# Performance work log

Hardware: AMD Instinct MI355X
Metric: run time of the kernel (lower is better)

Reference implementation:

```python
import jax, jax.numpy as jnp
import numpy as np

N = 100000   # nodes
E = 1600000  # edges (avg degree 16)
IN, H, HID, OUT = 128, 2, 64, 32


def setup_inputs() -> dict:
    key = jax.random.key(0)
    ks = jax.random.split(key, 20)
    def p(k, shape, scale=0.1):
        return jax.random.normal(k, shape, jnp.float32) * scale
    inp = {
        "x": jax.random.normal(ks[0], (N, IN), jnp.float32),
        "edge_index": jax.random.randint(ks[1], (2, E), 0, N),
    }
    # per-layer params: W [din, H*dout], att_src/att_dst [H, dout], bias
    dims = [(IN, HID), (H * HID, HID), (H * HID, HID), (H * HID, OUT)]
    for i, (din, dout) in enumerate(dims):
        inp[f"W{i}"] = p(ks[2 + 4 * i], (din, H * dout))
        inp[f"asrc{i}"] = p(ks[3 + 4 * i], (H, dout))
        inp[f"adst{i}"] = p(ks[4 + 4 * i], (H, dout))
        inp[f"b{i}"] = jnp.zeros((H * dout if i < 3 else dout,), jnp.float32)
    return inp


def gat_conv(h, src, dst, W, a_s, a_d, b, concat):
    # PyG GATConv, add_self_loops=False, negative_slope=0.2, eval mode
    heads, dout = a_s.shape
    n = h.shape[0]
    xl = (h @ W).reshape(n, heads, dout)              # [N, H, D]
    alpha_src = jnp.einsum('nhd,hd->nh', xl, a_s)     # [N, H]
    alpha_dst = jnp.einsum('nhd,hd->nh', xl, a_d)
    e = alpha_src[src] + alpha_dst[dst]               # [E, H]
    e = jax.nn.leaky_relu(e, 0.2)
    # segment softmax over edges sharing a destination node
    m = jax.ops.segment_max(e, dst, num_segments=n)
    m = jnp.where(jnp.isfinite(m), m, 0.0)            # guard isolated nodes
    ex = jnp.exp(e - m[dst])
    denom = jax.ops.segment_sum(ex, dst, num_segments=n)
    alpha = ex / (denom[dst] + 1e-16)                 # [E, H]
    msg = xl[src] * alpha[:, :, None]                 # [E, H, D]
    out = jax.ops.segment_sum(msg, dst, num_segments=n)
    out = out.reshape(n, heads * dout) if concat else out.mean(axis=1)
    return out + b


def reference(x, edge_index, W0, asrc0, adst0, b0, W1, asrc1, adst1, b1,
              W2, asrc2, adst2, b2, W3, asrc3, adst3, b3):
    src, dst = edge_index[0], edge_index[1]
    layers = [
        (W0, asrc0, adst0, b0, True),
        (W1, asrc1, adst1, b1, True),
        (W2, asrc2, adst2, b2, True),
        (W3, asrc3, adst3, b3, False),
    ]
    h = x
    for i, (W, a_s, a_d, b, concat) in enumerate(layers):
        h = gat_conv(h, src, dst, W, a_s, a_d, b, concat)
        if i != len(layers) - 1:
            h = jax.nn.relu(h)
    return jax.nn.log_softmax(h, axis=-1)
```

## Files before the change

### kernel.cpp

```cpp
#include <hip/hip_runtime.h>
#include <hip/hip_bf16.h>
#include <math.h>

#define N_NODES 100000
#define N_EDGES 1600000

constexpr int BSHIFT = 9, BMASK = 511;
constexpr int NBUCKET = (N_NODES + 511) / 512;
constexpr int BCAP = 16384;
constexpr int CAPB = 12288;
constexpr int EPT = 16, BIN_T = 256, BIN_CHUNK = BIN_T * EPT;

typedef __attribute__((ext_vector_type(8))) short bf16x8;
typedef __attribute__((ext_vector_type(4))) float f32x4;

__device__ __forceinline__ unsigned short f2bf(float f) {
    unsigned int u = __float_as_uint(f);
    unsigned int r = (u + 0x7fff + ((u >> 16) & 1)) >> 16;
    return (unsigned short)r;
}


__global__ __launch_bounds__(BIN_T) void bin_kernel(const int* __restrict__ src,
                                                    const int* __restrict__ dst,
                                                    int* __restrict__ bcnt,
                                                    unsigned int* __restrict__ bstore, int E) {
    __shared__ int cnt[NBUCKET];
    __shared__ int base[NBUCKET];
    int t = threadIdx.x;
    for (int i = t; i < NBUCKET; i += BIN_T) cnt[i] = 0;
    __syncthreads();
    int e0 = blockIdx.x * BIN_CHUNK;
    int ssrc[EPT], sdst[EPT];
#pragma unroll
    for (int k = 0; k < EPT; ++k) {
        int e = e0 + t + k * BIN_T;
        if (e < E) {
            ssrc[k] = src[e];
            sdst[k] = dst[e];
            atomicAdd(&cnt[sdst[k] >> BSHIFT], 1);
        } else {
            sdst[k] = -1;
        }
    }
    __syncthreads();
    for (int i = t; i < NBUCKET; i += BIN_T) {
        base[i] = atomicAdd(&bcnt[i], cnt[i]);
        cnt[i] = 0;
    }
    __syncthreads();
#pragma unroll
    for (int k = 0; k < EPT; ++k) {
        if (sdst[k] >= 0) {
            int b = sdst[k] >> BSHIFT;
            int off = base[b] + atomicAdd(&cnt[b], 1);
            if (off < BCAP)
                bstore[(size_t)b * BCAP + off] =
                    ((unsigned)ssrc[k] << BSHIFT) | (unsigned)(sdst[k] & BMASK);
        }
    }
}

__global__ __launch_bounds__(256) void scan_bcnt_kernel(const int* __restrict__ bcnt,
                                                        int* __restrict__ bbase) {
    __shared__ int sh[256];
    int t = threadIdx.x;
    int v = (t < NBUCKET) ? min(bcnt[t], BCAP) : 0;
    sh[t] = v;
    __syncthreads();
    for (int off = 1; off < 256; off <<= 1) {
        int x = (t >= off) ? sh[t - off] : 0;
        __syncthreads();
        sh[t] += x;
        __syncthreads();
    }
    if (t < NBUCKET) bbase[t + 1] = sh[t];
    if (t == 0) bbase[0] = 0;
}

__global__ __launch_bounds__(256) void build_col_v2(const int* __restrict__ bcnt,
                                                    const int* __restrict__ bbase,
                                                    const unsigned int* __restrict__ bstore,
                                                    int* __restrict__ rp, int* __restrict__ col,
                                                    int N) {
    __shared__ int sA[512], sB[512];
    __shared__ int lofs[513];
    __shared__ int colStage[CAPB];
    int b = blockIdx.x, t = threadIdx.x;
    int nodeBase = b << BSHIFT;
    int nNodes = min(512, N - nodeBase);
    for (int i = t; i < 512; i += 256) sA[i] = 0;
    __syncthreads();
    int cnt = min(bcnt[b], BCAP);
    size_t sbase = (size_t)b * BCAP;
    for (int i = t; i < cnt; i += 256) atomicAdd(&sA[bstore[sbase + i] & BMASK], 1);
    __syncthreads();
    int* srcp = sA; int* dstp = sB;
    for (int off = 1; off < 512; off <<= 1) {
        for (int i = t; i < 512; i += 256) dstp[i] = srcp[i] + ((i >= off) ? srcp[i - off] : 0);
        __syncthreads();
        int* tmp = srcp; srcp = dstp; dstp = tmp;
    }
    for (int i = t; i < 512; i += 256) lofs[i + 1] = srcp[i];
    if (t == 0) lofs[0] = 0;
    for (int i = t; i < 512; i += 256) dstp[i] = 0;
    __syncthreads();
    int gbase = bbase[b];
    for (int i = t; i < nNodes; i += 256) rp[nodeBase + i] = gbase + lofs[i];
    if (b == NBUCKET - 1 && t == 0) rp[N] = gbase + lofs[nNodes];
    for (int i = t; i < cnt; i += 256) {
        unsigned e = bstore[sbase + i];
        int dl = e & BMASK;
        int sv = (int)(e >> BSHIFT);
        int pos = lofs[dl] + atomicAdd(&dstp[dl], 1);
        if (pos < CAPB) colStage[pos] = sv;
        else col[gbase + pos] = sv;
    }
    __syncthreads();
    int lim = min(cnt, CAPB);
    for (int i = t; i < lim; i += 256) col[gbase + i] = colStage[i];
}

__global__ __launch_bounds__(256) void transpose_all_w(
    const float* __restrict__ W0, const float* __restrict__ W1,
    const float* __restrict__ W2, const float* __restrict__ W3,
    unsigned int* __restrict__ Wt0, unsigned int* __restrict__ Wt1,
    unsigned int* __restrict__ Wt2, unsigned int* __restrict__ Wt3) {
    int idx = blockIdx.x * 256 + threadIdx.x;
    const float* W; unsigned int* Wt; int C, base;
    if (idx < 8192)       { W = W0; Wt = Wt0; C = 128; base = 0; }
    else if (idx < 16384) { W = W1; Wt = Wt1; C = 128; base = 8192; }
    else if (idx < 24576) { W = W2; Wt = Wt2; C = 128; base = 16384; }
    else if (idx < 28672) { W = W3; Wt = Wt3; C = 64;  base = 24576; }
    else return;
    int l = idx - base;
    int c = l >> 6, kk = l & 63;
    float w0 = W[(2 * kk) * C + c];
    float w1 = W[(2 * kk + 1) * C + c];
    Wt[c * 64 + kk] = (unsigned)f2bf(w0) | ((unsigned)f2bf(w1) << 16);
}


template<int HD, bool F32IN>
__global__ __launch_bounds__(64) void gemm_alpha_mfma(
    const void* __restrict__ hsrc, const unsigned short* __restrict__ Wt,
    const float* __restrict__ a_s, const float* __restrict__ a_d,
    __hip_bfloat16* __restrict__ xl, float* __restrict__ asrc, float* __restrict__ adst) {
    constexpr int NT = HD / 16;
    constexpr int GR = HD / 4;
    int node0 = blockIdx.x * 16;
    int t = threadIdx.x;
    int lan = t & 15, grp = t >> 4;

    __shared__ float ob[16][HD + 4];

    bf16x8 af[4];
    if constexpr (F32IN) {
        __shared__ unsigned short hb[16][136];
        const float4* h4 = (const float4*)hsrc;
#pragma unroll
        for (int it = 0; it < 8; ++it) {
            int idx = it * 64 + t;
            int nn = idx >> 5, kk = idx & 31;
            float4 v = h4[(size_t)(node0 + nn) * 32 + kk];
            ushort4 u;
            u.x = f2bf(v.x); u.y = f2bf(v.y); u.z = f2bf(v.z); u.w = f2bf(v.w);
            *(ushort4*)&hb[nn][kk * 4] = u;
        }
        __syncthreads();
#pragma unroll
        for (int ks = 0; ks < 4; ++ks)
            af[ks] = *(const bf16x8*)&hb[lan][ks * 32 + grp * 8];
    } else {
        const unsigned short* hbf = (const unsigned short*)hsrc;
#pragma unroll
        for (int ks = 0; ks < 4; ++ks)
            af[ks] = *(const bf16x8*)(hbf + (size_t)(node0 + lan) * 128 + ks * 32 + grp * 8);
    }

    f32x4 acc[NT];
#pragma unroll
    for (int i = 0; i < NT; ++i) acc[i] = (f32x4){0.f, 0.f, 0.f, 0.f};

#pragma unroll
    for (int ks = 0; ks < 4; ++ks) {
        bf16x8 bfr[NT];
#pragma unroll
        for (int nt = 0; nt < NT; ++nt)
            bfr[nt] = *(const bf16x8*)(Wt + (size_t)(nt * 16 + lan) * 128 + ks * 32 + grp * 8);
#pragma unroll
        for (int nt = 0; nt < NT; ++nt)
            acc[nt] = __builtin_amdgcn_mfma_f32_16x16x32_bf16(af[ks], bfr[nt], acc[nt], 0, 0, 0);
    }

    float av[NT], dv[NT];
#pragma unroll
    for (int nt = 0; nt < NT; ++nt) {
        av[nt] = a_s[nt * 16 + lan];
        dv[nt] = a_d[nt * 16 + lan];
    }
    float psum[2][4] = {{0.f,0.f,0.f,0.f},{0.f,0.f,0.f,0.f}};
    float pdum[2][4] = {{0.f,0.f,0.f,0.f},{0.f,0.f,0.f,0.f}};
#pragma unroll
    for (int nt = 0; nt < NT; ++nt) {
        int hs = (nt >= NT / 2) ? 1 : 0;
#pragma unroll
        for (int j = 0; j < 4; ++j) {
            psum[hs][j] = fmaf(acc[nt][j], av[nt], psum[hs][j]);
            pdum[hs][j] = fmaf(acc[nt][j], dv[nt], pdum[hs][j]);
        }
    }
#pragma unroll
    for (int off = 1; off <= 8; off <<= 1) {
#pragma unroll
        for (int hs = 0; hs < 2; ++hs)
#pragma unroll
            for (int j = 0; j < 4; ++j) {
                psum[hs][j] += __shfl_xor(psum[hs][j], off, 64);
                pdum[hs][j] += __shfl_xor(pdum[hs][j], off, 64);
            }
    }
    if (lan == 0) {
#pragma unroll
        for (int j = 0; j < 4; ++j) {
            int node = node0 + grp * 4 + j;
            asrc[node * 2 + 0] = psum[0][j];
            asrc[node * 2 + 1] = psum[1][j];
            adst[node * 2 + 0] = pdum[0][j];
            adst[node * 2 + 1] = pdum[1][j];
        }
    }

#pragma unroll
    for (int nt = 0; nt < NT; ++nt)
#pragma unroll
        for (int j = 0; j < 4; ++j)
            ob[grp * 4 + j][nt * 16 + lan] = acc[nt][j];
    __syncthreads();
#pragma unroll
    for (int it = 0; it < 16 * GR / 64; ++it) {
        int idx = it * 64 + t;
        int nn = idx / GR, g = idx % GR;
        float4 v = *(const float4*)&ob[nn][g * 4];
        uint2 u;
        u.x = (unsigned)f2bf(v.x) | ((unsigned)f2bf(v.y) << 16);
        u.y = (unsigned)f2bf(v.z) | ((unsigned)f2bf(v.w) << 16);
        ((uint2*)xl)[(size_t)(node0 + nn) * GR + g] = u;
    }
}


__global__ void aggregate_relu_v5(const __hip_bfloat162* __restrict__ xl2,
                                  const float2* __restrict__ a_src, const float2* __restrict__ a_dst,
                                  const int* __restrict__ rp, const int* __restrict__ col,
                                  const float* __restrict__ bias, unsigned int* __restrict__ out) {
    int node = blockIdx.x;
    int t = threadIdx.x;
    int head = t >> 5;
    int beg = rp[node], deg = rp[node + 1] - beg;
    float2 adn = a_dst[node];

    __shared__ int   snS[64];
    __shared__ float pS[2][64];

    float s0 = 0.f, s1 = 0.f;
    float ax0 = 0.f, ay0 = 0.f, ax1 = 0.f, ay1 = 0.f;
    float ax2 = 0.f, ay2 = 0.f, ax3 = 0.f, ay3 = 0.f;

    if (deg <= 64) {
        float e0 = -INFINITY, e1 = -INFINITY;
        if (t < deg) {
            int sn = col[beg + t];
            snS[t] = sn;
            float2 a = a_src[sn];
            e0 = a.x + adn.x; e0 = (e0 >= 0.f) ? e0 : 0.2f * e0;
            e1 = a.y + adn.y; e1 = (e1 >= 0.f) ? e1 : 0.2f * e1;
        }
        float m0 = e0, m1 = e1;
#pragma unroll
        for (int off = 32; off >= 1; off >>= 1) {
            m0 = fmaxf(m0, __shfl_xor(m0, off, 64));
            m1 = fmaxf(m1, __shfl_xor(m1, off, 64));
        }
        if (t < deg) {
            float p0 = __expf(e0 - m0), p1 = __expf(e1 - m1);
            pS[0][t] = p0; pS[1][t] = p1;
            s0 = p0; s1 = p1;
        }
        __syncthreads();
        int j = 0;
        for (; j + 8 <= deg; j += 8) {
            int sa = snS[j+0], sb = snS[j+1], sc = snS[j+2], sd = snS[j+3];
            int se = snS[j+4], sf = snS[j+5], sg = snS[j+6], sh = snS[j+7];
            float pa = pS[head][j+0], pb = pS[head][j+1], pc = pS[head][j+2], pd = pS[head][j+3];
            float pe = pS[head][j+4], pf = pS[head][j+5], pg = pS[head][j+6], ph = pS[head][j+7];
            __hip_bfloat162 va = xl2[(size_t)sa * 64 + t];
            __hip_bfloat162 vb = xl2[(size_t)sb * 64 + t];
            __hip_bfloat162 vc = xl2[(size_t)sc * 64 + t];
            __hip_bfloat162 vd = xl2[(size_t)sd * 64 + t];
            __hip_bfloat162 ve = xl2[(size_t)se * 64 + t];
            __hip_bfloat162 vf = xl2[(size_t)sf * 64 + t];
            __hip_bfloat162 vg = xl2[(size_t)sg * 64 + t];
            __hip_bfloat162 vh = xl2[(size_t)sh * 64 + t];
            ax0 = fmaf(pa, __bfloat162float(va.x), ax0); ay0 = fmaf(pa, __bfloat162float(va.y), ay0);
            ax1 = fmaf(pb, __bfloat162float(vb.x), ax1); ay1 = fmaf(pb, __bfloat162float(vb.y), ay1);
            ax2 = fmaf(pc, __bfloat162float(vc.x), ax2); ay2 = fmaf(pc, __bfloat162float(vc.y), ay2);
            ax3 = fmaf(pd, __bfloat162float(vd.x), ax3); ay3 = fmaf(pd, __bfloat162float(vd.y), ay3);
            ax0 = fmaf(pe, __bfloat162float(ve.x), ax0); ay0 = fmaf(pe, __bfloat162float(ve.y), ay0);
            ax1 = fmaf(pf, __bfloat162float(vf.x), ax1); ay1 = fmaf(pf, __bfloat162float(vf.y), ay1);
            ax2 = fmaf(pg, __bfloat162float(vg.x), ax2); ay2 = fmaf(pg, __bfloat162float(vg.y), ay2);
            ax3 = fmaf(ph, __bfloat162float(vh.x), ax3); ay3 = fmaf(ph, __bfloat162float(vh.y), ay3);
        }
        for (; j < deg; ++j) {
            int sn = snS[j];
            float p = pS[head][j];
            __hip_bfloat162 v = xl2[(size_t)sn * 64 + t];
            ax0 = fmaf(p, __bfloat162float(v.x), ax0);
            ay0 = fmaf(p, __bfloat162float(v.y), ay0);
        }
    } else {
        float m0 = -INFINITY, m1 = -INFINITY;
        for (int j = t; j < deg; j += 64) {
            float2 a = a_src[col[beg + j]];
            float e0 = a.x + adn.x; e0 = (e0 >= 0.f) ? e0 : 0.2f * e0;
            float e1 = a.y + adn.y; e1 = (e1 >= 0.f) ? e1 : 0.2f * e1;
            m0 = fmaxf(m0, e0); m1 = fmaxf(m1, e1);
        }
#pragma unroll
        for (int off = 32; off >= 1; off >>= 1) {
            m0 = fmaxf(m0, __shfl_xor(m0, off, 64));
            m1 = fmaxf(m1, __shfl_xor(m1, off, 64));
        }
        for (int c0 = 0; c0 < deg; c0 += 64) {
            int csz = min(64, deg - c0);
            if (t < csz) {
                int sn = col[beg + c0 + t];
                float2 a = a_src[sn];
                float e0 = a.x + adn.x; e0 = (e0 >= 0.f) ? e0 : 0.2f * e0;
                float e1 = a.y + adn.y; e1 = (e1 >= 0.f) ? e1 : 0.2f * e1;
                float p0 = __expf(e0 - m0), p1 = __expf(e1 - m1);
                snS[t] = sn; pS[0][t] = p0; pS[1][t] = p1;
                s0 += p0; s1 += p1;
            }
            __syncthreads();
            for (int j = 0; j < csz; ++j) {
                int sn = snS[j];
                float p = pS[head][j];
                __hip_bfloat162 v = xl2[(size_t)sn * 64 + t];
                ax0 = fmaf(p, __bfloat162float(v.x), ax0);
                ay0 = fmaf(p, __bfloat162float(v.y), ay0);
            }
            __syncthreads();
        }
    }
#pragma unroll
    for (int off = 32; off >= 1; off >>= 1) {
        s0 += __shfl_xor(s0, off, 64);
        s1 += __shfl_xor(s1, off, 64);
    }
    float s = head ? s1 : s0;
    float inv = 1.0f / (s + 1e-16f);
    float2 b2 = ((const float2*)bias)[t];
    float ox = fmaxf(fmaf(ax0 + ax1 + ax2 + ax3, inv, b2.x), 0.f);
    float oy = fmaxf(fmaf(ay0 + ay1 + ay2 + ay3, inv, b2.y), 0.f);
    out[(size_t)node * 64 + t] = (unsigned)f2bf(ox) | ((unsigned)f2bf(oy) << 16);
}

__global__ void aggregate_final_v4(const __hip_bfloat16* __restrict__ xl,
                                   const float2* __restrict__ a_src, const float2* __restrict__ a_dst,
                                   const int* __restrict__ rp, const int* __restrict__ col,
                                   const float* __restrict__ bias, float* __restrict__ out) {
    int node = blockIdx.x;
    int t = threadIdx.x;
    int head = t >> 5;
    int beg = rp[node], deg = rp[node + 1] - beg;
    float2 adn = a_dst[node];

    __shared__ int   snS[64];
    __shared__ float pS[2][64];

    float s0 = 0.f, s1 = 0.f;
    float a0 = 0.f, a1 = 0.f, a2 = 0.f, a3 = 0.f;

    if (deg <= 64) {
        float e0 = -INFINITY, e1 = -INFINITY;
        if (t < deg) {
            int sn = col[beg + t];
            snS[t] = sn;
            float2 a = a_src[sn];
            e0 = a.x + adn.x; e0 = (e0 >= 0.f) ? e0 : 0.2f * e0;
            e1 = a.y + adn.y; e1 = (e1 >= 0.f) ? e1 : 0.2f * e1;
        }
        float m0 = e0, m1 = e1;
#pragma unroll
        for (int off = 32; off >= 1; off >>= 1) {
            m0 = fmaxf(m0, __shfl_xor(m0, off, 64));
            m1 = fmaxf(m1, __shfl_xor(m1, off, 64));
        }
        if (t < deg) {
            float p0 = __expf(e0 - m0), p1 = __expf(e1 - m1);
            pS[0][t] = p0; pS[1][t] = p1;
            s0 = p0; s1 = p1;
        }
        __syncthreads();
        int j = 0;
        for (; j + 8 <= deg; j += 8) {
            int sa = snS[j+0], sb = snS[j+1], sc = snS[j+2], sd = snS[j+3];
            int se = snS[j+4], sf = snS[j+5], sg = snS[j+6], sh = snS[j+7];
            float pa = pS[head][j+0], pb = pS[head][j+1], pc = pS[head][j+2], pd = pS[head][j+3];
            float pe = pS[head][j+4], pf = pS[head][j+5], pg = pS[head][j+6], ph = pS[head][j+7];
            float va = __bfloat162float(xl[(size_t)sa * 64 + t]);
            float vb = __bfloat162float(xl[(size_t)sb * 64 + t]);
            float vc = __bfloat162float(xl[(size_t)sc * 64 + t]);
            float vd = __bfloat162float(xl[(size_t)sd * 64 + t]);
            float ve = __bfloat162float(xl[(size_t)se * 64 + t]);
            float vf = __bfloat162float(xl[(size_t)sf * 64 + t]);
            float vg = __bfloat162float(xl[(size_t)sg * 64 + t]);
            float vh = __bfloat162float(xl[(size_t)sh * 64 + t]);
            a0 = fmaf(pa, va, a0); a1 = fmaf(pb, vb, a1);
            a2 = fmaf(pc, vc, a2); a3 = fmaf(pd, vd, a3);
            a0 = fmaf(pe, ve, a0); a1 = fmaf(pf, vf, a1);
            a2 = fmaf(pg, vg, a2); a3 = fmaf(ph, vh, a3);
        }
        for (; j < deg; ++j) {
            a0 = fmaf(pS[head][j], __bfloat162float(xl[(size_t)snS[j] * 64 + t]), a0);
        }
    } else {
        float m0 = -INFINITY, m1 = -INFINITY;
        for (int j = t; j < deg; j += 64) {
            float2 a = a_src[col[beg + j]];
            float e0 = a.x + adn.x; e0 = (e0 >= 0.f) ? e0 : 0.2f * e0;
            float e1 = a.y + adn.y; e1 = (e1 >= 0.f) ? e1 : 0.2f * e1;
            m0 = fmaxf(m0, e0); m1 = fmaxf(m1, e1);
        }
#pragma unroll
        for (int off = 32; off >= 1; off >>= 1) {
            m0 = fmaxf(m0, __shfl_xor(m0, off, 64));
            m1 = fmaxf(m1, __shfl_xor(m1, off, 64));
        }
        for (int c0 = 0; c0 < deg; c0 += 64) {
            int csz = min(64, deg - c0);
            if (t < csz) {
                int sn = col[beg + c0 + t];
                float2 a = a_src[sn];
                float e0 = a.x + adn.x; e0 = (e0 >= 0.f) ? e0 : 0.2f * e0;
                float e1 = a.y + adn.y; e1 = (e1 >= 0.f) ? e1 : 0.2f * e1;
                float p0 = __expf(e0 - m0), p1 = __expf(e1 - m1);
                snS[t] = sn; pS[0][t] = p0; pS[1][t] = p1;
                s0 += p0; s1 += p1;
            }
            __syncthreads();
            for (int j = 0; j < csz; ++j) {
                a0 = fmaf(pS[head][j], __bfloat162float(xl[(size_t)snS[j] * 64 + t]), a0);
            }
            __syncthreads();
        }
    }
#pragma unroll
    for (int off = 32; off >= 1; off >>= 1) {
        s0 += __shfl_xor(s0, off, 64);
        s1 += __shfl_xor(s1, off, 64);
    }
    float s = head ? s1 : s0;
    float o = (a0 + a1 + a2 + a3) / (s + 1e-16f);
    float other = __shfl_down(o, 32, 64);
    if (t < 32) {
        float v = 0.5f * (o + other) + bias[t];
        float mx = v;
#pragma unroll
        for (int off = 16; off >= 1; off >>= 1) mx = fmaxf(mx, __shfl_xor(mx, off, 32));
        float ex = __expf(v - mx);
        float sm = ex;
#pragma unroll
        for (int off = 16; off >= 1; off >>= 1) sm += __shfl_xor(sm, off, 32);
        out[(size_t)node * 32 + t] = v - mx - logf(sm);
    }
}


extern "C" void kernel_launch(void* const* d_in, const int* in_sizes, int n_in,
                              void* d_out, int out_size, void* d_ws, size_t ws_size,
                              hipStream_t stream) {
    const int N = N_NODES, E = N_EDGES;

    const float* x  = (const float*)d_in[0];
    const int*  ei  = (const int*)d_in[1];
    const float* W0 = (const float*)d_in[2];
    const float* as0 = (const float*)d_in[3];
    const float* ad0 = (const float*)d_in[4];
    const float* b0 = (const float*)d_in[5];
    const float* W1 = (const float*)d_in[6];
    const float* as1 = (const float*)d_in[7];
    const float* ad1 = (const float*)d_in[8];
    const float* b1 = (const float*)d_in[9];
    const float* W2 = (const float*)d_in[10];
    const float* as2 = (const float*)d_in[11];
    const float* ad2 = (const float*)d_in[12];
    const float* b2 = (const float*)d_in[13];
    const float* W3 = (const float*)d_in[14];
    const float* as3 = (const float*)d_in[15];
    const float* ad3 = (const float*)d_in[16];
    const float* b3 = (const float*)d_in[17];
    float* out = (float*)d_out;

    const int* srcv = ei;
    const int* dstv = ei + E;

    char* p = (char*)d_ws;
    auto carve = [&](size_t bytes) -> void* {
        void* r = (void*)p;
        p += (bytes + 255) & ~(size_t)255;
        return r;
    };
    int* rp       = (int*)carve((size_t)(N + 1) * 4);
    int* col      = (int*)carve((size_t)E * 4);
    int* bcnt     = (int*)carve((size_t)NBUCKET * 4);
    int* bbase    = (int*)carve((size_t)(NBUCKET + 1) * 4);
    unsigned int* bstore = (unsigned int*)carve((size_t)NBUCKET * BCAP * 4);
    __hip_bfloat16* bufX = (__hip_bfloat16*)carve((size_t)N * 128 * 2);
    __hip_bfloat16* bufH = (__hip_bfloat16*)carve((size_t)N * 128 * 2);
    float* asrc   = (float*)carve((size_t)N * 2 * 4);
    float* adst   = (float*)carve((size_t)N * 2 * 4);
    unsigned short* Wt0 = (unsigned short*)carve((size_t)128 * 128 * 2);
    unsigned short* Wt1 = (unsigned short*)carve((size_t)128 * 128 * 2);
    unsigned short* Wt2 = (unsigned short*)carve((size_t)128 * 128 * 2);
    unsigned short* Wt3 = (unsigned short*)carve((size_t)64 * 128 * 2);

    hipMemsetAsync(bcnt, 0, (size_t)NBUCKET * 4, stream);

    transpose_all_w<<<112, 256, 0, stream>>>(W0, W1, W2, W3,
                                             (unsigned int*)Wt0, (unsigned int*)Wt1,
                                             (unsigned int*)Wt2, (unsigned int*)Wt3);

    bin_kernel<<<(E + BIN_CHUNK - 1) / BIN_CHUNK, BIN_T, 0, stream>>>(srcv, dstv, bcnt, bstore, E);
    scan_bcnt_kernel<<<1, 256, 0, stream>>>(bcnt, bbase);
    build_col_v2<<<NBUCKET, 256, 0, stream>>>(bcnt, bbase, bstore, rp, col, N);

    const __hip_bfloat162* bufX2 = (const __hip_bfloat162*)bufX;
    const float2* asrc2 = (const float2*)asrc;
    const float2* adst2 = (const float2*)adst;

    gemm_alpha_mfma<128, true><<<N / 16, 64, 0, stream>>>(x, Wt0, as0, ad0, bufX, asrc, adst);
    aggregate_relu_v5<<<N, 64, 0, stream>>>(bufX2, asrc2, adst2, rp, col, b0, (unsigned int*)bufH);
    gemm_alpha_mfma<128, false><<<N / 16, 64, 0, stream>>>(bufH, Wt1, as1, ad1, bufX, asrc, adst);
    aggregate_relu_v5<<<N, 64, 0, stream>>>(bufX2, asrc2, adst2, rp, col, b1, (unsigned int*)bufH);
    gemm_alpha_mfma<128, false><<<N / 16, 64, 0, stream>>>(bufH, Wt2, as2, ad2, bufX, asrc, adst);
    aggregate_relu_v5<<<N, 64, 0, stream>>>(bufX2, asrc2, adst2, rp, col, b2, (unsigned int*)bufH);
    gemm_alpha_mfma<64, false><<<N / 16, 64, 0, stream>>>(bufH, Wt3, as3, ad3, bufX, asrc, adst);
    aggregate_final_v4<<<N, 64, 0, stream>>>(bufX, asrc2, adst2, rp, col, b3, out);
}
```

Before: 532.7 us.

## Fold attention dot products into GEMM weights and merge bucket scan into column build

Precomputes W·a_src and W·a_dst per head as four extra weight columns (plus zero padding to a full MFMA tile), so the attention logits come out of one additional MFMA tile rather than a per-block FMA and shuffle reduction. Separately, the one-block bucket-count scan is folded into the column-build kernel, where every block redoes the 256-entry scan, removing one launch. The cost is an extra MFMA tile and extra weight loads per GEMM block, and the attention logits now come from bf16-rounded fused weights, which changes their precision.

Measured after the change: 557.8 us. 1.05x slower.

```diff
diff --git a/kernel.cpp b/kernel.cpp
--- a/kernel.cpp
+++ b/kernel.cpp
@@ -61,32 +61,26 @@
     }
 }
 
-__global__ __launch_bounds__(256) void scan_bcnt_kernel(const int* __restrict__ bcnt,
-                                                        int* __restrict__ bbase) {
-    __shared__ int sh[256];
-    int t = threadIdx.x;
-    int v = (t < NBUCKET) ? min(bcnt[t], BCAP) : 0;
-    sh[t] = v;
-    __syncthreads();
-    for (int off = 1; off < 256; off <<= 1) {
-        int x = (t >= off) ? sh[t - off] : 0;
-        __syncthreads();
-        sh[t] += x;
-        __syncthreads();
-    }
-    if (t < NBUCKET) bbase[t + 1] = sh[t];
-    if (t == 0) bbase[0] = 0;
-}
-
-__global__ __launch_bounds__(256) void build_col_v2(const int* __restrict__ bcnt,
-                                                    const int* __restrict__ bbase,
+__global__ __launch_bounds__(256) void build_col_v3(const int* __restrict__ bcnt,
                                                     const unsigned int* __restrict__ bstore,
                                                     int* __restrict__ rp, int* __restrict__ col,
                                                     int N) {
+    __shared__ int sc[256];
     __shared__ int sA[512], sB[512];
     __shared__ int lofs[513];
     __shared__ int colStage[CAPB];
     int b = blockIdx.x, t = threadIdx.x;
+    int v = (t < NBUCKET) ? min(bcnt[t], BCAP) : 0;
+    sc[t] = v;
+    __syncthreads();
+    for (int off = 1; off < 256; off <<= 1) {
+        int x = (t >= off) ? sc[t - off] : 0;
+        __syncthreads();
+        sc[t] += x;
+        __syncthreads();
+    }
+    int gbase = (b == 0) ? 0 : sc[b - 1];
+
     int nodeBase = b << BSHIFT;
     int nNodes = min(512, N - nodeBase);
     for (int i = t; i < 512; i += 256) sA[i] = 0;
@@ -105,7 +99,6 @@
     if (t == 0) lofs[0] = 0;
     for (int i = t; i < 512; i += 256) dstp[i] = 0;
     __syncthreads();
-    int gbase = bbase[b];
     for (int i = t; i < nNodes; i += 256) rp[nodeBase + i] = gbase + lofs[i];
     if (b == NBUCKET - 1 && t == 0) rp[N] = gbase + lofs[nNodes];
     for (int i = t; i < cnt; i += 256) {
@@ -140,11 +133,38 @@
     Wt[c * 64 + kk] = (unsigned)f2bf(w0) | ((unsigned)f2bf(w1) << 16);
 }
 
+__global__ __launch_bounds__(512) void fuse_dots(
+    const float* __restrict__ W0, const float* __restrict__ W1,
+    const float* __restrict__ W2, const float* __restrict__ W3,
+    const float* __restrict__ as0, const float* __restrict__ ad0,
+    const float* __restrict__ as1, const float* __restrict__ ad1,
+    const float* __restrict__ as2, const float* __restrict__ ad2,
+    const float* __restrict__ as3, const float* __restrict__ ad3,
+    unsigned short* __restrict__ Wt0, unsigned short* __restrict__ Wt1,
+    unsigned short* __restrict__ Wt2, unsigned short* __restrict__ Wt3) {
+    int l = blockIdx.x;
+    int t = threadIdx.x;
+    const float* W  = (l == 0) ? W0 : (l == 1) ? W1 : (l == 2) ? W2 : W3;
+    const float* as = (l == 0) ? as0 : (l == 1) ? as1 : (l == 2) ? as2 : as3;
+    const float* ad = (l == 0) ? ad0 : (l == 1) ? ad1 : (l == 2) ? ad2 : ad3;
+    unsigned short* Wt = (l == 0) ? Wt0 : (l == 1) ? Wt1 : (l == 2) ? Wt2 : Wt3;
+    int C = (l < 3) ? 128 : 64;
+    int dout = C / 2;
+    int k = t & 127, v = t >> 7;
+    int head = v & 1;
+    const float* a = (v >> 1) ? ad : as;
+    float s = 0.f;
+    for (int d = 0; d < dout; ++d)
+        s += W[k * C + head * dout + d] * a[head * dout + d];
+    Wt[(C + v) * 128 + k] = f2bf(s);
+    int padBase = (C + 4) * 128;
+    for (int i = t; i < 12 * 128; i += 512) Wt[padBase + i] = 0;
+}
+
 
 template<int HD, bool F32IN>
 __global__ __launch_bounds__(64) void gemm_alpha_mfma(
     const void* __restrict__ hsrc, const unsigned short* __restrict__ Wt,
-    const float* __restrict__ a_s, const float* __restrict__ a_d,
     __hip_bfloat16* __restrict__ xl, float* __restrict__ asrc, float* __restrict__ adst) {
     constexpr int NT = HD / 16;
     constexpr int GR = HD / 4;
@@ -178,56 +198,28 @@
             af[ks] = *(const bf16x8*)(hbf + (size_t)(node0 + lan) * 128 + ks * 32 + grp * 8);
     }
 
-    f32x4 acc[NT];
-#pragma unroll
-    for (int i = 0; i < NT; ++i) acc[i] = (f32x4){0.f, 0.f, 0.f, 0.f};
+    f32x4 acc[NT + 1];
+#pragma unroll
+    for (int i = 0; i <= NT; ++i) acc[i] = (f32x4){0.f, 0.f, 0.f, 0.f};
 
 #pragma unroll
     for (int ks = 0; ks < 4; ++ks) {
-        bf16x8 bfr[NT];
-#pragma unroll
-        for (int nt = 0; nt < NT; ++nt)
+        bf16x8 bfr[NT + 1];
+#pragma unroll
+        for (int nt = 0; nt <= NT; ++nt)
             bfr[nt] = *(const bf16x8*)(Wt + (size_t)(nt * 16 + lan) * 128 + ks * 32 + grp * 8);
 #pragma unroll
-        for (int nt = 0; nt < NT; ++nt)
+        for (int nt = 0; nt <= NT; ++nt)
             acc[nt] = __builtin_amdgcn_mfma_f32_16x16x32_bf16(af[ks], bfr[nt], acc[nt], 0, 0, 0);
     }
 
-    float av[NT], dv[NT];
-#pragma unroll
-    for (int nt = 0; nt < NT; ++nt) {
-        av[nt] = a_s[nt * 16 + lan];
-        dv[nt] = a_d[nt * 16 + lan];
-    }
-    float psum[2][4] = {{0.f,0.f,0.f,0.f},{0.f,0.f,0.f,0.f}};
-    float pdum[2][4] = {{0.f,0.f,0.f,0.f},{0.f,0.f,0.f,0.f}};
-#pragma unroll
-    for (int nt = 0; nt < NT; ++nt) {
-        int hs = (nt >= NT / 2) ? 1 : 0;
-#pragma unroll
-        for (int j = 0; j < 4; ++j) {
-            psum[hs][j] = fmaf(acc[nt][j], av[nt], psum[hs][j]);
-            pdum[hs][j] = fmaf(acc[nt][j], dv[nt], pdum[hs][j]);
-        }
-    }
-#pragma unroll
-    for (int off = 1; off <= 8; off <<= 1) {
-#pragma unroll
-        for (int hs = 0; hs < 2; ++hs)
-#pragma unroll
-            for (int j = 0; j < 4; ++j) {
-                psum[hs][j] += __shfl_xor(psum[hs][j], off, 64);
-                pdum[hs][j] += __shfl_xor(pdum[hs][j], off, 64);
-            }
-    }
-    if (lan == 0) {
+    if (lan < 4) {
+        float* dst = (lan < 2) ? asrc : adst;
+        int hh = lan & 1;
 #pragma unroll
         for (int j = 0; j < 4; ++j) {
             int node = node0 + grp * 4 + j;
-            asrc[node * 2 + 0] = psum[0][j];
-            asrc[node * 2 + 1] = psum[1][j];
-            adst[node * 2 + 0] = pdum[0][j];
-            adst[node * 2 + 1] = pdum[1][j];
+            dst[node * 2 + hh] = acc[NT][j];
         }
     }
 
@@ -515,37 +507,38 @@
     int* rp       = (int*)carve((size_t)(N + 1) * 4);
     int* col      = (int*)carve((size_t)E * 4);
     int* bcnt     = (int*)carve((size_t)NBUCKET * 4);
-    int* bbase    = (int*)carve((size_t)(NBUCKET + 1) * 4);
     unsigned int* bstore = (unsigned int*)carve((size_t)NBUCKET * BCAP * 4);
     __hip_bfloat16* bufX = (__hip_bfloat16*)carve((size_t)N * 128 * 2);
     __hip_bfloat16* bufH = (__hip_bfloat16*)carve((size_t)N * 128 * 2);
     float* asrc   = (float*)carve((size_t)N * 2 * 4);
     float* adst   = (float*)carve((size_t)N * 2 * 4);
-    unsigned short* Wt0 = (unsigned short*)carve((size_t)128 * 128 * 2);
-    unsigned short* Wt1 = (unsigned short*)carve((size_t)128 * 128 * 2);
-    unsigned short* Wt2 = (unsigned short*)carve((size_t)128 * 128 * 2);
-    unsigned short* Wt3 = (unsigned short*)carve((size_t)64 * 128 * 2);
+    unsigned short* Wt0 = (unsigned short*)carve((size_t)144 * 128 * 2);
+    unsigned short* Wt1 = (unsigned short*)carve((size_t)144 * 128 * 2);
+    unsigned short* Wt2 = (unsigned short*)carve((size_t)144 * 128 * 2);
+    unsigned short* Wt3 = (unsigned short*)carve((size_t)80 * 128 * 2);
 
     hipMemsetAsync(bcnt, 0, (size_t)NBUCKET * 4, stream);
 
     transpose_all_w<<<112, 256, 0, stream>>>(W0, W1, W2, W3,
                                              (unsigned int*)Wt0, (unsigned int*)Wt1,
                                              (unsigned int*)Wt2, (unsigned int*)Wt3);
+    fuse_dots<<<4, 512, 0, stream>>>(W0, W1, W2, W3,
+                                     as0, ad0, as1, ad1, as2, ad2, as3, ad3,
+                                     Wt0, Wt1, Wt2, Wt3);
 
     bin_kernel<<<(E + BIN_CHUNK - 1) / BIN_CHUNK, BIN_T, 0, stream>>>(srcv, dstv, bcnt, bstore, E);
-    scan_bcnt_kernel<<<1, 256, 0, stream>>>(bcnt, bbase);
-    build_col_v2<<<NBUCKET, 256, 0, stream>>>(bcnt, bbase, bstore, rp, col, N);
+    build_col_v3<<<NBUCKET, 256, 0, stream>>>(bcnt, bstore, rp, col, N);
 
     const __hip_bfloat162* bufX2 = (const __hip_bfloat162*)bufX;
     const float2* asrc2 = (const float2*)asrc;
     const float2* adst2 = (const float2*)adst;
 
-    gemm_alpha_mfma<128, true><<<N / 16, 64, 0, stream>>>(x, Wt0, as0, ad0, bufX, asrc, adst);
+    gemm_alpha_mfma<128, true><<<N / 16, 64, 0, stream>>>(x, Wt0, bufX, asrc, adst);
     aggregate_relu_v5<<<N, 64, 0, stream>>>(bufX2, asrc2, adst2, rp, col, b0, (unsigned int*)bufH);
-    gemm_alpha_mfma<128, false><<<N / 16, 64, 0, stream>>>(bufH, Wt1, as1, ad1, bufX, asrc, adst);
+    gemm_alpha_mfma<128, false><<<N / 16, 64, 0, stream>>>(bufH, Wt1, bufX, asrc, adst);
     aggregate_relu_v5<<<N, 64, 0, stream>>>(bufX2, asrc2, adst2, rp, col, b1, (unsigned int*)bufH);
-    gemm_alpha_mfma<128, false><<<N / 16, 64, 0, stream>>>(bufH, Wt2, as2, ad2, bufX, asrc, adst);
+    gemm_alpha_mfma<128, false><<<N / 16, 64, 0, stream>>>(bufH, Wt2, bufX, asrc, adst);
     aggregate_relu_v5<<<N, 64, 0, stream>>>(bufX2, asrc2, adst2, rp, col, b2, (unsigned int*)bufH);
-    gemm_alpha_mfma<64, false><<<N / 16, 64, 0, stream>>>(bufH, Wt3, as3, ad3, bufX, asrc, adst);
+    gemm_alpha_mfma<64, false><<<N / 16, 64, 0, stream>>>(bufH, Wt3, bufX, asrc, adst);
     aggregate_final_v4<<<N, 64, 0, stream>>>(bufX, asrc2, adst2, rp, col, b3, out);
 }
```
